# Performance work log

Measured on AMD Instinct MI355X. Metric: run time of the kernel, lower is better.

Reference implementation:

```python
import jax, jax.numpy as jnp
import numpy as np

ITERATION = 3
NEG = -2.0**16 + 1.0  # mask fill value from the torch code


def setup_inputs() -> dict:
    key = jax.random.key(0)
    k1, k2, k3, k4 = jax.random.split(key, 4)
    B, L, D_in, D_out, K = 1024, 512, 64, 64, 8
    low_capsule = jax.random.normal(k1, (B, L, D_in), dtype=jnp.float32)
    B_init = jax.random.normal(k2, (1, K, L), dtype=jnp.float32)
    S = jax.random.normal(k3, (D_in, D_out), dtype=jnp.float32)
    seq_len = jax.random.randint(k4, (B, 1), 1, L + 1, dtype=jnp.int32)
    return {"low_capsule": low_capsule, "B_init": B_init, "S": S, "seq_len": seq_len}


def _squash(x):
    # torch code sums squared norm over dim=1 (the capsule/max_k dim), keepdim
    sq = jnp.sum(jnp.square(x), axis=1, keepdims=True)
    scale = sq / (1.0 + sq) / jnp.sqrt(sq + 1e-9)
    return scale * x


def reference(low_capsule, B_init, S, seq_len):
    # low_capsule: [B, L, D_in], B_init: [1, K, L], S: [D_in, D_out], seq_len: [B, 1]
    Bsz, L, _ = low_capsule.shape
    K = B_init.shape[1]
    # sequence mask: [B, K, L] (seq_len tiled over K)
    mask = jnp.arange(L, dtype=seq_len.dtype)[None, None, :] < seq_len[:, :, None]
    mask = jnp.broadcast_to(mask, (Bsz, K, L))
    # bilinear projection is loop-invariant; compute once
    low_new = jnp.einsum('bld,do->blo', low_capsule, S)  # [B, L, D_out]
    B_mat = B_init
    high = None
    for _ in range(ITERATION):
        logits = jnp.where(mask, B_mat, NEG)               # [B, K, L]
        W = jax.nn.softmax(logits, axis=-1)                # masked softmax
        high = _squash(jnp.einsum('bkl,blo->bko', W, low_new))  # [B, K, D_out]
        B_delta = jnp.sum(jnp.einsum('bko,blo->bkl', high, low_new),
                          axis=0, keepdims=True)           # [1, K, L]
        B_mat = B_mat + B_delta
    return high
```

## Files before the change

kernel.cpp:

```cpp
#include <hip/hip_runtime.h>

#define NEG_FILL (-65535.0f)
#define NSLOT 32

typedef __attribute__((ext_vector_type(8))) short  short8;
typedef __attribute__((ext_vector_type(4))) float  floatx4;

__device__ inline unsigned short f2bf(float f) {
    unsigned u = __float_as_uint(f);
    u += 0x7FFFu + ((u >> 16) & 1u);
    return (unsigned short)(u >> 16);
}
__device__ inline float bf2f(unsigned short h) {
    return __uint_as_float(((unsigned)h) << 16);
}

__global__ __launch_bounds__(256) void k_init(const float* __restrict__ Binit,
                                              float* __restrict__ B0,
                                              float* __restrict__ slots) {
    int i = blockIdx.x * 256 + threadIdx.x;
    slots[i] = 0.f;
    if (i < 4096) B0[i] = Binit[i];
}

__global__ __launch_bounds__(256) void k_bred(const float* __restrict__ Bcur,
                                              float* __restrict__ Bnext,
                                              float* __restrict__ slots) {
    int i = blockIdx.x * 256 + threadIdx.x;
    float s = Bcur[i];
    #pragma unroll
    for (int j = 0; j < NSLOT; ++j) {
        s += slots[j * 4096 + i];
        slots[j * 4096 + i] = 0.f;
    }
    Bnext[i] = s;
}

__device__ __forceinline__ void softmax_to_WsT(
    const float* __restrict__ Bc, int sl, int lane, int g,
    float (*WsT)[8]) {
    #pragma unroll
    for (int kk = 0; kk < 2; ++kk) {
        const int k = g + (kk << 2);
        float v[8];
        float mx = NEG_FILL;
        #pragma unroll
        for (int j = 0; j < 8; ++j) {
            int l = lane + (j << 6);
            v[j] = (l < sl) ? Bc[(k << 9) + l] : NEG_FILL;
            mx = fmaxf(mx, v[j]);
        }
        #pragma unroll
        for (int off = 32; off; off >>= 1) mx = fmaxf(mx, __shfl_xor(mx, off));
        float s = 0.f;
        #pragma unroll
        for (int j = 0; j < 8; ++j) { v[j] = expf(v[j] - mx); s += v[j]; }
        #pragma unroll
        for (int off = 32; off; off >>= 1) s += __shfl_xor(s, off);
        const float inv = 1.0f / s;
        #pragma unroll
        for (int j = 0; j < 8; ++j) WsT[lane + (j << 6)][k] = v[j] * inv;
    }
}

__device__ __forceinline__ void delta_phase(
    const unsigned short* __restrict__ lnb, const unsigned short (*Hn)[64],
    float* __restrict__ slot, int g, int m, int q) {
    short8 afragH[2];
    #pragma unroll
    for (int oh = 0; oh < 2; ++oh) {
        short8 f = {0, 0, 0, 0, 0, 0, 0, 0};
        if (m < 8) f = *(const short8*)&Hn[m][oh * 32 + q * 8];
        afragH[oh] = f;
    }
    #pragma unroll
    for (int half = 0; half < 2; ++half) {
        short8 bf[4][2];
        #pragma unroll
        for (int t2 = 0; t2 < 4; ++t2) {
            const int lt = (g << 7) + (((half << 2) + t2) << 4);
            const unsigned short* p = &lnb[((lt + m) << 6) + q * 8];
            bf[t2][0] = *(const short8*)p;
            bf[t2][1] = *(const short8*)(p + 32);
        }
        #pragma unroll
        for (int t2 = 0; t2 < 4; ++t2) {
            const int lt = (g << 7) + (((half << 2) + t2) << 4);
            floatx4 acc = {0.f, 0.f, 0.f, 0.f};
            acc = __builtin_amdgcn_mfma_f32_16x16x32_bf16(afragH[0], bf[t2][0], acc, 0, 0, 0);
            acc = __builtin_amdgcn_mfma_f32_16x16x32_bf16(afragH[1], bf[t2][1], acc, 0, 0, 0);
            if (q < 2) {
                #pragma unroll
                for (int r = 0; r < 4; ++r)
                    atomicAdd(&slot[(q * 4 + r) * 512 + lt + m], acc[r]);
            }
        }
    }
}

__global__ __launch_bounds__(256, 4) void k_fused0(
    const float* __restrict__ low,
    const float* __restrict__ S,
    const float* __restrict__ Bc,
    float* __restrict__ slots,
    const int* __restrict__ seq_len,
    unsigned short* __restrict__ ln)
{
    __shared__ __align__(16) float WsT[512][8];
    __shared__ __align__(16) float Tpart[4][8][64];
    __shared__ __align__(16) float Tred[8][64];
    __shared__ __align__(16) unsigned short Hn[8][64];

    const int t = threadIdx.x, lane = t & 63, g = t >> 6, b = blockIdx.x;
    const int m = lane & 15, q = lane >> 4;
    const int sl = seq_len[b];
    const float* lowb = low + ((size_t)b << 15);
    unsigned short* lnb = ln + ((size_t)b << 15);

    softmax_to_WsT(Bc, sl, lane, g, WsT);
    __syncthreads();

    short8 sfrag[4][2];
    #pragma unroll
    for (int nt = 0; nt < 4; ++nt)
        #pragma unroll
        for (int dh = 0; dh < 2; ++dh) {
            short8 f;
            #pragma unroll
            for (int j = 0; j < 8; ++j) {
                int d = dh * 32 + q * 8 + j;
                f[j] = (short)f2bf(S[(d << 6) + nt * 16 + m]);
            }
            sfrag[nt][dh] = f;
        }

    float Tp[8][4];
    #pragma unroll
    for (int k = 0; k < 8; ++k)
        #pragma unroll
        for (int nt = 0; nt < 4; ++nt) Tp[k][nt] = 0.f;

    for (int tt = 0; tt < 8; ++tt) {
        const int lt = (g << 7) + (tt << 4);
        short8 afrag[2];
        #pragma unroll
        for (int dh = 0; dh < 2; ++dh) {
            const float4* p =
                (const float4*)&lowb[((lt + m) << 6) + dh * 32 + q * 8];
            float4 x0 = p[0], x1 = p[1];
            short8 f;
            f[0] = (short)f2bf(x0.x); f[1] = (short)f2bf(x0.y);
            f[2] = (short)f2bf(x0.z); f[3] = (short)f2bf(x0.w);
            f[4] = (short)f2bf(x1.x); f[5] = (short)f2bf(x1.y);
            f[6] = (short)f2bf(x1.z); f[7] = (short)f2bf(x1.w);
            afrag[dh] = f;
        }
        float lnr[4][4];
        #pragma unroll
        for (int nt = 0; nt < 4; ++nt) {
            floatx4 acc = {0.f, 0.f, 0.f, 0.f};
            acc = __builtin_amdgcn_mfma_f32_16x16x32_bf16(afrag[0], sfrag[nt][0], acc, 0, 0, 0);
            acc = __builtin_amdgcn_mfma_f32_16x16x32_bf16(afrag[1], sfrag[nt][1], acc, 0, 0, 0);
            #pragma unroll
            for (int r = 0; r < 4; ++r) {
                unsigned short hb = f2bf(acc[r]);
                lnb[((size_t)(lt + (q << 2) + r) << 6) + nt * 16 + m] = hb;
                lnr[r][nt] = bf2f(hb);
            }
        }
        #pragma unroll
        for (int r = 0; r < 4; ++r) {
            const int l = lt + (q << 2) + r;
            const float4 wa = *(const float4*)&WsT[l][0];
            const float4 wb = *(const float4*)&WsT[l][4];
            #pragma unroll
            for (int nt = 0; nt < 4; ++nt) {
                const float x = lnr[r][nt];
                Tp[0][nt] = fmaf(wa.x, x, Tp[0][nt]);
                Tp[1][nt] = fmaf(wa.y, x, Tp[1][nt]);
                Tp[2][nt] = fmaf(wa.z, x, Tp[2][nt]);
                Tp[3][nt] = fmaf(wa.w, x, Tp[3][nt]);
                Tp[4][nt] = fmaf(wb.x, x, Tp[4][nt]);
                Tp[5][nt] = fmaf(wb.y, x, Tp[5][nt]);
                Tp[6][nt] = fmaf(wb.z, x, Tp[6][nt]);
                Tp[7][nt] = fmaf(wb.w, x, Tp[7][nt]);
            }
        }
    }
    #pragma unroll
    for (int k = 0; k < 8; ++k)
        #pragma unroll
        for (int nt = 0; nt < 4; ++nt) {
            float v = Tp[k][nt];
            v += __shfl_xor(v, 16);
            v += __shfl_xor(v, 32);
            Tp[k][nt] = v;
        }
    #pragma unroll
    for (int k = 0; k < 8; ++k) Tpart[g][k][lane] = Tp[k][q];
    __syncthreads();

    #pragma unroll
    for (int idx = t; idx < 512; idx += 256) {
        float s = (&Tpart[0][0][0])[idx] + (&Tpart[1][0][0])[idx]
                + (&Tpart[2][0][0])[idx] + (&Tpart[3][0][0])[idx];
        (&Tred[0][0])[idx] = s;
    }
    __syncthreads();

    float sq = 0.f;
    #pragma unroll
    for (int k = 0; k < 8; ++k) { float x = Tred[k][lane]; sq = fmaf(x, x, sq); }
    const float scale = sq / (1.0f + sq) / sqrtf(sq + 1e-9f);
    Hn[g][lane]     = f2bf(scale * Tred[g][lane]);
    Hn[g + 4][lane] = f2bf(scale * Tred[g + 4][lane]);
    __syncthreads();

    delta_phase(lnb, Hn, slots + ((size_t)(b & (NSLOT - 1)) << 12), g, m, q);
}

__global__ __launch_bounds__(256, 4) void k_route2(
    const unsigned short* __restrict__ ln,
    const float* __restrict__ Bc,
    float* __restrict__ slots,
    const int* __restrict__ seq_len,
    float* __restrict__ out,
    int last)
{
    __shared__ __align__(16) float WsT[512][8];
    __shared__ __align__(16) float Tpart[4][8][64];
    __shared__ __align__(16) float Tred[8][64];
    __shared__ __align__(16) unsigned short Hn[8][64];

    const int t = threadIdx.x, lane = t & 63, g = t >> 6, b = blockIdx.x;
    const int m = lane & 15, q = lane >> 4;
    const int sl = seq_len[b];
    const unsigned short* lnb = ln + ((size_t)b << 15);

    softmax_to_WsT(Bc, sl, lane, g, WsT);
    __syncthreads();

    floatx4 Tacc[8];
    #pragma unroll
    for (int k = 0; k < 8; ++k) Tacc[k] = (floatx4){0.f, 0.f, 0.f, 0.f};
    const int l0 = g << 7;
    for (int ii = 0; ii < 4; ++ii) {
        uint2 u[8];
        #pragma unroll
        for (int j = 0; j < 8; ++j) {
            const int l = l0 + (ii << 5) + (j << 2) + q;
            u[j] = *(const uint2*)&lnb[(l << 6) + (m << 2)];
        }
        #pragma unroll
        for (int j = 0; j < 8; ++j) {
            const int l = l0 + (ii << 5) + (j << 2) + q;
            const float x0 = __uint_as_float(u[j].x << 16);
            const float x1 = __uint_as_float(u[j].x & 0xFFFF0000u);
            const float x2 = __uint_as_float(u[j].y << 16);
            const float x3 = __uint_as_float(u[j].y & 0xFFFF0000u);
            const float4 wa = *(const float4*)&WsT[l][0];
            const float4 wb = *(const float4*)&WsT[l][4];
#define TROW(K, WV)                                          \
            Tacc[K][0] = fmaf(WV, x0, Tacc[K][0]);           \
            Tacc[K][1] = fmaf(WV, x1, Tacc[K][1]);           \
            Tacc[K][2] = fmaf(WV, x2, Tacc[K][2]);           \
            Tacc[K][3] = fmaf(WV, x3, Tacc[K][3]);
            TROW(0, wa.x) TROW(1, wa.y) TROW(2, wa.z) TROW(3, wa.w)
            TROW(4, wb.x) TROW(5, wb.y) TROW(6, wb.z) TROW(7, wb.w)
#undef TROW
        }
    }
    #pragma unroll
    for (int k = 0; k < 8; ++k)
        #pragma unroll
        for (int j = 0; j < 4; ++j) {
            float v = Tacc[k][j];
            v += __shfl_xor(v, 16);
            v += __shfl_xor(v, 32);
            Tacc[k][j] = v;
        }
    if (q == 0) {
        #pragma unroll
        for (int k = 0; k < 8; ++k)
            *(float4*)&Tpart[g][k][m << 2] =
                make_float4(Tacc[k][0], Tacc[k][1], Tacc[k][2], Tacc[k][3]);
    }
    __syncthreads();

    #pragma unroll
    for (int idx = t; idx < 512; idx += 256) {
        float s = (&Tpart[0][0][0])[idx] + (&Tpart[1][0][0])[idx]
                + (&Tpart[2][0][0])[idx] + (&Tpart[3][0][0])[idx];
        (&Tred[0][0])[idx] = s;
    }
    __syncthreads();

    float sq = 0.f;
    #pragma unroll
    for (int k = 0; k < 8; ++k) { float x = Tred[k][lane]; sq = fmaf(x, x, sq); }
    const float scale = sq / (1.0f + sq) / sqrtf(sq + 1e-9f);
    const float hf0 = scale * Tred[g][lane];
    const float hf1 = scale * Tred[g + 4][lane];

    if (last) {
        out[(((size_t)b * 8 + g)     << 6) + lane] = hf0;
        out[(((size_t)b * 8 + g + 4) << 6) + lane] = hf1;
        return;
    }
    Hn[g][lane]     = f2bf(hf0);
    Hn[g + 4][lane] = f2bf(hf1);
    __syncthreads();

    delta_phase(lnb, Hn, slots + ((size_t)(b & (NSLOT - 1)) << 12), g, m, q);
}

__global__ __launch_bounds__(256) void k_copy4k(const float* __restrict__ src,
                                                float* __restrict__ dst) {
    int i = blockIdx.x * 256 + threadIdx.x;
    dst[i] = src[i];
}

__global__ __launch_bounds__(256, 4) void k_route(
    const float* __restrict__ low, const float* __restrict__ S,
    const float* __restrict__ Bcur, float* __restrict__ Bnext,
    const int* __restrict__ seq_len, float* __restrict__ out, int last)
{
    __shared__ float smemA[64 * 65];
    __shared__ float Spad[64][65];
    __shared__ float GT[64][8];
    __shared__ float Tred[8][64];
    float* WsT = smemA;
    float (*Tpart)[8][64] = (float (*)[8][64])smemA;
    float (*tile)[65]     = (float (*)[65])smemA;

    const int t = threadIdx.x, o = t & 63, g = t >> 6, b = blockIdx.x;
    const int sl = seq_len[b];
    const float* lowb = low + ((size_t)b << 15);

    #pragma unroll
    for (int i = 0; i < 16; ++i) {
        int idx = t + (i << 8);
        Spad[idx >> 6][idx & 63] = S[idx];
    }
    #pragma unroll
    for (int kk = 0; kk < 2; ++kk) {
        const int k = g + (kk << 2);
        float v[8];
        float mx = NEG_FILL;
        #pragma unroll
        for (int j = 0; j < 8; ++j) {
            int l = o + (j << 6);
            v[j] = (l < sl) ? Bcur[(k << 9) + l] : NEG_FILL;
            mx = fmaxf(mx, v[j]);
        }
        #pragma unroll
        for (int off = 32; off; off >>= 1) mx = fmaxf(mx, __shfl_xor(mx, off));
        float s = 0.f;
        #pragma unroll
        for (int j = 0; j < 8; ++j) { v[j] = expf(v[j] - mx); s += v[j]; }
        #pragma unroll
        for (int off = 32; off; off >>= 1) s += __shfl_xor(s, off);
        const float inv = 1.0f / s;
        #pragma unroll
        for (int j = 0; j < 8; ++j) WsT[((o + (j << 6)) << 3) + k] = v[j] * inv;
    }
    __syncthreads();

    float Ta[8];
    #pragma unroll
    for (int k = 0; k < 8; ++k) Ta[k] = 0.f;
    {
        const int l0 = g << 7;
        #pragma unroll 4
        for (int i = 0; i < 128; ++i) {
            const int l = l0 + i;
            const float x = lowb[(l << 6) + o];
            const float4 wa = *(const float4*)&WsT[(l << 3)];
            const float4 wb = *(const float4*)&WsT[(l << 3) + 4];
            Ta[0] = fmaf(wa.x, x, Ta[0]); Ta[1] = fmaf(wa.y, x, Ta[1]);
            Ta[2] = fmaf(wa.z, x, Ta[2]); Ta[3] = fmaf(wa.w, x, Ta[3]);
            Ta[4] = fmaf(wb.x, x, Ta[4]); Ta[5] = fmaf(wb.y, x, Ta[5]);
            Ta[6] = fmaf(wb.z, x, Ta[6]); Ta[7] = fmaf(wb.w, x, Ta[7]);
        }
    }
    __syncthreads();
    #pragma unroll
    for (int k = 0; k < 8; ++k) Tpart[g][k][o] = Ta[k];
    __syncthreads();

    float h0 = 0.f, h1 = 0.f;
    #pragma unroll
    for (int gg = 0; gg < 4; ++gg) { h0 += Tpart[gg][g][o]; h1 += Tpart[gg][g + 4][o]; }
    Tred[g][o] = h0; Tred[g + 4][o] = h1;
    __syncthreads();

    float hp0 = 0.f, hp1 = 0.f;
    #pragma unroll
    for (int d = 0; d < 64; ++d) {
        const float sv = Spad[d][o];
        hp0 = fmaf(Tred[g][d], sv, hp0);
        hp1 = fmaf(Tred[g + 4][d], sv, hp1);
    }
    __syncthreads();
    Tred[g][o] = hp0; Tred[g + 4][o] = hp1;
    __syncthreads();

    float sq = 0.f;
    #pragma unroll
    for (int k = 0; k < 8; ++k) { float x = Tred[k][o]; sq = fmaf(x, x, sq); }
    const float scale = sq / (1.0f + sq) / sqrtf(sq + 1e-9f);
    const float hf0 = scale * hp0;
    const float hf1 = scale * hp1;

    if (last) {
        out[(((size_t)b * 8 + g)     << 6) + o] = hf0;
        out[(((size_t)b * 8 + g + 4) << 6) + o] = hf1;
        return;
    }
    __syncthreads();
    Tred[g][o] = hf0; Tred[g + 4][o] = hf1;
    __syncthreads();

    float g0 = 0.f, g1 = 0.f;
    #pragma unroll
    for (int oo = 0; oo < 64; ++oo) {
        const float sv = Spad[o][oo];
        g0 = fmaf(Tred[g][oo], sv, g0);
        g1 = fmaf(Tred[g + 4][oo], sv, g1);
    }
    GT[o][g] = g0; GT[o][g + 4] = g1;
    __syncthreads();

    for (int c = 0; c < 8; ++c) {
        const int lc = c << 6;
        #pragma unroll
        for (int r = 0; r < 16; ++r) {
            const int lr = (g << 4) + r;
            tile[lr][o] = lowb[((lc + lr) << 6) + o];
        }
        __syncthreads();
        float a0 = 0.f, a1 = 0.f;
        #pragma unroll
        for (int d = 0; d < 64; ++d) {
            const float x = tile[o][d];
            a0 = fmaf(GT[d][g], x, a0);
            a1 = fmaf(GT[d][g + 4], x, a1);
        }
        atomicAdd(&Bnext[(g << 9) + lc + o], a0);
        atomicAdd(&Bnext[((g + 4) << 9) + lc + o], a1);
        __syncthreads();
    }
}

extern "C" void kernel_launch(void* const* d_in, const int* in_sizes, int n_in,
                              void* d_out, int out_size, void* d_ws, size_t ws_size,
                              hipStream_t stream) {
    const float* low   = (const float*)d_in[0];
    const float* Binit = (const float*)d_in[1];
    const float* S     = (const float*)d_in[2];
    const int*   seq   = (const int*)d_in[3];
    float* outp = (float*)d_out;

    const size_t LN_BYTES   = (size_t)1024 * 512 * 64 * 2;
    const size_t SLOT_BYTES = (size_t)NSLOT * 4096 * sizeof(float);
    const size_t NEED = LN_BYTES + SLOT_BYTES + 2 * 4096 * sizeof(float);

    if (ws_size >= NEED) {
        unsigned short* lnw = (unsigned short*)d_ws;
        float* slots = (float*)((char*)d_ws + LN_BYTES);
        float* B0 = slots + (size_t)NSLOT * 4096;
        float* B1 = B0 + 4096;

        k_init<<<(NSLOT * 4096) / 256, 256, 0, stream>>>(Binit, B0, slots);

        k_fused0<<<1024, 256, 0, stream>>>(low, S, B0, slots, seq, lnw);
        k_bred<<<16, 256, 0, stream>>>(B0, B1, slots);

        k_route2<<<1024, 256, 0, stream>>>(lnw, B1, slots, seq, outp, 0);
        k_bred<<<16, 256, 0, stream>>>(B1, B0, slots);

        k_route2<<<1024, 256, 0, stream>>>(lnw, B0, nullptr, seq, outp, 1);
    } else {
        float* B0 = (float*)d_ws;
        float* B1 = B0 + 4096;
        k_copy4k<<<16, 256, 0, stream>>>(Binit, B0);
        k_copy4k<<<16, 256, 0, stream>>>(B0, B1);
        k_route<<<1024, 256, 0, stream>>>(low, S, B0, B1, seq, outp, 0);
        k_copy4k<<<16, 256, 0, stream>>>(B1, B0);
        k_route<<<1024, 256, 0, stream>>>(low, S, B1, B0, seq, outp, 0);
        k_route<<<1024, 256, 0, stream>>>(low, S, B0, nullptr, seq, outp, 1);
    }
}
```

Measured before the change: 283.3 us.

## Split each batch row across two blocks and separate delta into its own kernel

Each batch row's routing work is now split across two blocks, each handling half of the sequence. Partial T sums are atomically accumulated into a global buffer that reuses the output array. The squash and delta MFMA phase moves into a separate k_delta kernel, and a final k_out kernel applies the squash. This doubles the block count and lowers per-block shared memory (launch bounds raised to 6) for better occupancy, at the cost of extra kernel launches, global atomics, and T-buffer zeroing traffic in k_bred.

After: 373.4 us. 1.32x slower.

```diff
diff --git a/kernel.cpp b/kernel.cpp
--- a/kernel.cpp
+++ b/kernel.cpp
@@ -15,17 +15,17 @@
     return __uint_as_float(((unsigned)h) << 16);
 }
 
-__global__ __launch_bounds__(256) void k_init(const float* __restrict__ Binit,
-                                              float* __restrict__ B0,
-                                              float* __restrict__ slots) {
+__global__ __launch_bounds__(256) void k_init(float* __restrict__ slots,
+                                              float* __restrict__ Tbuf) {
     int i = blockIdx.x * 256 + threadIdx.x;
-    slots[i] = 0.f;
-    if (i < 4096) B0[i] = Binit[i];
+    Tbuf[i] = 0.f;
+    if (i < NSLOT * 4096) slots[i] = 0.f;
 }
 
 __global__ __launch_bounds__(256) void k_bred(const float* __restrict__ Bcur,
                                               float* __restrict__ Bnext,
-                                              float* __restrict__ slots) {
+                                              float* __restrict__ slots,
+                                              float* __restrict__ Tbuf) {
     int i = blockIdx.x * 256 + threadIdx.x;
     float s = Bcur[i];
     #pragma unroll
@@ -34,10 +34,12 @@
         slots[j * 4096 + i] = 0.f;
     }
     Bnext[i] = s;
-}
-
-__device__ __forceinline__ void softmax_to_WsT(
-    const float* __restrict__ Bc, int sl, int lane, int g,
+    #pragma unroll 16
+    for (int j = 0; j < 128; ++j) Tbuf[j * 4096 + i] = 0.f;
+}
+
+__device__ __forceinline__ void softmax_half(
+    const float* __restrict__ Bc, int sl, int lane, int g, int half,
     float (*WsT)[8]) {
     #pragma unroll
     for (int kk = 0; kk < 2; ++kk) {
@@ -59,65 +61,30 @@
         for (int off = 32; off; off >>= 1) s += __shfl_xor(s, off);
         const float inv = 1.0f / s;
         #pragma unroll
-        for (int j = 0; j < 8; ++j) WsT[lane + (j << 6)][k] = v[j] * inv;
-    }
-}
-
-__device__ __forceinline__ void delta_phase(
-    const unsigned short* __restrict__ lnb, const unsigned short (*Hn)[64],
-    float* __restrict__ slot, int g, int m, int q) {
-    short8 afragH[2];
-    #pragma unroll
-    for (int oh = 0; oh < 2; ++oh) {
-        short8 f = {0, 0, 0, 0, 0, 0, 0, 0};
-        if (m < 8) f = *(const short8*)&Hn[m][oh * 32 + q * 8];
-        afragH[oh] = f;
-    }
-    #pragma unroll
-    for (int half = 0; half < 2; ++half) {
-        short8 bf[4][2];
-        #pragma unroll
-        for (int t2 = 0; t2 < 4; ++t2) {
-            const int lt = (g << 7) + (((half << 2) + t2) << 4);
-            const unsigned short* p = &lnb[((lt + m) << 6) + q * 8];
-            bf[t2][0] = *(const short8*)p;
-            bf[t2][1] = *(const short8*)(p + 32);
-        }
-        #pragma unroll
-        for (int t2 = 0; t2 < 4; ++t2) {
-            const int lt = (g << 7) + (((half << 2) + t2) << 4);
-            floatx4 acc = {0.f, 0.f, 0.f, 0.f};
-            acc = __builtin_amdgcn_mfma_f32_16x16x32_bf16(afragH[0], bf[t2][0], acc, 0, 0, 0);
-            acc = __builtin_amdgcn_mfma_f32_16x16x32_bf16(afragH[1], bf[t2][1], acc, 0, 0, 0);
-            if (q < 2) {
-                #pragma unroll
-                for (int r = 0; r < 4; ++r)
-                    atomicAdd(&slot[(q * 4 + r) * 512 + lt + m], acc[r]);
-            }
-        }
-    }
-}
-
-__global__ __launch_bounds__(256, 4) void k_fused0(
+        for (int j = 0; j < 4; ++j)
+            WsT[lane + (j << 6)][k] = v[(half << 2) + j] * inv;
+    }
+}
+
+__global__ __launch_bounds__(256, 6) void k_F0(
     const float* __restrict__ low,
     const float* __restrict__ S,
     const float* __restrict__ Bc,
-    float* __restrict__ slots,
     const int* __restrict__ seq_len,
-    unsigned short* __restrict__ ln)
+    unsigned short* __restrict__ ln,
+    float* __restrict__ Tbuf)
 {
-    __shared__ __align__(16) float WsT[512][8];
+    __shared__ __align__(16) float WsT[256][8];
     __shared__ __align__(16) float Tpart[4][8][64];
-    __shared__ __align__(16) float Tred[8][64];
-    __shared__ __align__(16) unsigned short Hn[8][64];
-
-    const int t = threadIdx.x, lane = t & 63, g = t >> 6, b = blockIdx.x;
+
+    const int t = threadIdx.x, lane = t & 63, g = t >> 6;
+    const int b = blockIdx.x >> 1, half = blockIdx.x & 1;
     const int m = lane & 15, q = lane >> 4;
     const int sl = seq_len[b];
-    const float* lowb = low + ((size_t)b << 15);
-    unsigned short* lnb = ln + ((size_t)b << 15);
-
-    softmax_to_WsT(Bc, sl, lane, g, WsT);
+    const float* lowb = low + ((size_t)b << 15) + ((size_t)half << 14);
+    unsigned short* lnb = ln + ((size_t)b << 15) + ((size_t)half << 14);
+
+    softmax_half(Bc, sl, lane, g, half, WsT);
     __syncthreads();
 
     short8 sfrag[4][2];
@@ -140,8 +107,8 @@
         #pragma unroll
         for (int nt = 0; nt < 4; ++nt) Tp[k][nt] = 0.f;
 
-    for (int tt = 0; tt < 8; ++tt) {
-        const int lt = (g << 7) + (tt << 4);
+    for (int tt = 0; tt < 4; ++tt) {
+        const int lt = (g << 6) + (tt << 4);
         short8 afrag[2];
         #pragma unroll
         for (int dh = 0; dh < 2; ++dh) {
@@ -155,18 +122,13 @@
             f[6] = (short)f2bf(x1.z); f[7] = (short)f2bf(x1.w);
             afrag[dh] = f;
         }
-        float lnr[4][4];
+        floatx4 accs[4];
         #pragma unroll
         for (int nt = 0; nt < 4; ++nt) {
             floatx4 acc = {0.f, 0.f, 0.f, 0.f};
             acc = __builtin_amdgcn_mfma_f32_16x16x32_bf16(afrag[0], sfrag[nt][0], acc, 0, 0, 0);
             acc = __builtin_amdgcn_mfma_f32_16x16x32_bf16(afrag[1], sfrag[nt][1], acc, 0, 0, 0);
-            #pragma unroll
-            for (int r = 0; r < 4; ++r) {
-                unsigned short hb = f2bf(acc[r]);
-                lnb[((size_t)(lt + (q << 2) + r) << 6) + nt * 16 + m] = hb;
-                lnr[r][nt] = bf2f(hb);
-            }
+            accs[nt] = acc;
         }
         #pragma unroll
         for (int r = 0; r < 4; ++r) {
@@ -175,7 +137,9 @@
             const float4 wb = *(const float4*)&WsT[l][4];
             #pragma unroll
             for (int nt = 0; nt < 4; ++nt) {
-                const float x = lnr[r][nt];
+                unsigned short hb = f2bf(accs[nt][r]);
+                lnb[((size_t)l << 6) + nt * 16 + m] = hb;
+                const float x = bf2f(hb);
                 Tp[0][nt] = fmaf(wa.x, x, Tp[0][nt]);
                 Tp[1][nt] = fmaf(wa.y, x, Tp[1][nt]);
                 Tp[2][nt] = fmaf(wa.z, x, Tp[2][nt]);
@@ -204,47 +168,33 @@
     for (int idx = t; idx < 512; idx += 256) {
         float s = (&Tpart[0][0][0])[idx] + (&Tpart[1][0][0])[idx]
                 + (&Tpart[2][0][0])[idx] + (&Tpart[3][0][0])[idx];
-        (&Tred[0][0])[idx] = s;
-    }
-    __syncthreads();
-
-    float sq = 0.f;
-    #pragma unroll
-    for (int k = 0; k < 8; ++k) { float x = Tred[k][lane]; sq = fmaf(x, x, sq); }
-    const float scale = sq / (1.0f + sq) / sqrtf(sq + 1e-9f);
-    Hn[g][lane]     = f2bf(scale * Tred[g][lane]);
-    Hn[g + 4][lane] = f2bf(scale * Tred[g + 4][lane]);
-    __syncthreads();
-
-    delta_phase(lnb, Hn, slots + ((size_t)(b & (NSLOT - 1)) << 12), g, m, q);
-}
-
-__global__ __launch_bounds__(256, 4) void k_route2(
+        atomicAdd(&Tbuf[((size_t)b << 9) + idx], s);
+    }
+}
+
+__global__ __launch_bounds__(256, 6) void k_T(
     const unsigned short* __restrict__ ln,
     const float* __restrict__ Bc,
-    float* __restrict__ slots,
     const int* __restrict__ seq_len,
-    float* __restrict__ out,
-    int last)
+    float* __restrict__ Tbuf)
 {
-    __shared__ __align__(16) float WsT[512][8];
+    __shared__ __align__(16) float WsT[256][8];
     __shared__ __align__(16) float Tpart[4][8][64];
-    __shared__ __align__(16) float Tred[8][64];
-    __shared__ __align__(16) unsigned short Hn[8][64];
-
-    const int t = threadIdx.x, lane = t & 63, g = t >> 6, b = blockIdx.x;
+
+    const int t = threadIdx.x, lane = t & 63, g = t >> 6;
+    const int b = blockIdx.x >> 1, half = blockIdx.x & 1;
     const int m = lane & 15, q = lane >> 4;
     const int sl = seq_len[b];
-    const unsigned short* lnb = ln + ((size_t)b << 15);
-
-    softmax_to_WsT(Bc, sl, lane, g, WsT);
+    const unsigned short* lnb = ln + ((size_t)b << 15) + ((size_t)half << 14);
+
+    softmax_half(Bc, sl, lane, g, half, WsT);
     __syncthreads();
 
     floatx4 Tacc[8];
     #pragma unroll
     for (int k = 0; k < 8; ++k) Tacc[k] = (floatx4){0.f, 0.f, 0.f, 0.f};
-    const int l0 = g << 7;
-    for (int ii = 0; ii < 4; ++ii) {
+    const int l0 = g << 6;
+    for (int ii = 0; ii < 2; ++ii) {
         uint2 u[8];
         #pragma unroll
         for (int j = 0; j < 8; ++j) {
@@ -291,27 +241,79 @@
     for (int idx = t; idx < 512; idx += 256) {
         float s = (&Tpart[0][0][0])[idx] + (&Tpart[1][0][0])[idx]
                 + (&Tpart[2][0][0])[idx] + (&Tpart[3][0][0])[idx];
-        (&Tred[0][0])[idx] = s;
-    }
-    __syncthreads();
-
-    float sq = 0.f;
-    #pragma unroll
-    for (int k = 0; k < 8; ++k) { float x = Tred[k][lane]; sq = fmaf(x, x, sq); }
+        atomicAdd(&Tbuf[((size_t)b << 9) + idx], s);
+    }
+}
+
+__global__ __launch_bounds__(256, 6) void k_delta(
+    const unsigned short* __restrict__ ln,
+    const float* __restrict__ Tbuf,
+    float* __restrict__ slots)
+{
+    __shared__ __align__(16) float Tl[512];
+    __shared__ __align__(16) unsigned short Hn[8][64];
+
+    const int t = threadIdx.x, lane = t & 63, g = t >> 6;
+    const int b = blockIdx.x >> 1, half = blockIdx.x & 1;
+    const int m = lane & 15, q = lane >> 4;
+    const unsigned short* lnb = ln + ((size_t)b << 15);
+    float* slot = slots + ((size_t)(b & (NSLOT - 1)) << 12);
+
+    Tl[t]       = Tbuf[((size_t)b << 9) + t];
+    Tl[t + 256] = Tbuf[((size_t)b << 9) + t + 256];
+    __syncthreads();
+    if (t < 64) {
+        float sq = 0.f;
+        #pragma unroll
+        for (int k = 0; k < 8; ++k) { float x = Tl[(k << 6) + t]; sq = fmaf(x, x, sq); }
+        const float scale = sq / (1.0f + sq) / sqrtf(sq + 1e-9f);
+        #pragma unroll
+        for (int k = 0; k < 8; ++k) Hn[k][t] = f2bf(scale * Tl[(k << 6) + t]);
+    }
+    __syncthreads();
+
+    short8 aH[2];
+    #pragma unroll
+    for (int oh = 0; oh < 2; ++oh) {
+        short8 f = {0, 0, 0, 0, 0, 0, 0, 0};
+        if (m < 8) f = *(const short8*)&Hn[m][oh * 32 + q * 8];
+        aH[oh] = f;
+    }
+    short8 bf[4][2];
+    #pragma unroll
+    for (int t2 = 0; t2 < 4; ++t2) {
+        const int lt = (half << 8) + (g << 6) + (t2 << 4);
+        const unsigned short* p = &lnb[((lt + m) << 6) + q * 8];
+        bf[t2][0] = *(const short8*)p;
+        bf[t2][1] = *(const short8*)(p + 32);
+    }
+    #pragma unroll
+    for (int t2 = 0; t2 < 4; ++t2) {
+        const int lt = (half << 8) + (g << 6) + (t2 << 4);
+        floatx4 acc = {0.f, 0.f, 0.f, 0.f};
+        acc = __builtin_amdgcn_mfma_f32_16x16x32_bf16(aH[0], bf[t2][0], acc, 0, 0, 0);
+        acc = __builtin_amdgcn_mfma_f32_16x16x32_bf16(aH[1], bf[t2][1], acc, 0, 0, 0);
+        if (q < 2) {
+            #pragma unroll
+            for (int r = 0; r < 4; ++r)
+                atomicAdd(&slot[((q << 2) + r) * 512 + lt + m], acc[r]);
+        }
+    }
+}
+
+__global__ __launch_bounds__(256) void k_out(float* T_io) {
+    const int idx = blockIdx.x * 256 + threadIdx.x;
+    const int b = idx >> 6, o = idx & 63;
+    float v[8]; float sq = 0.f;
+    #pragma unroll
+    for (int k = 0; k < 8; ++k) {
+        v[k] = T_io[((size_t)b << 9) + (k << 6) + o];
+        sq = fmaf(v[k], v[k], sq);
+    }
     const float scale = sq / (1.0f + sq) / sqrtf(sq + 1e-9f);
-    const float hf0 = scale * Tred[g][lane];
-    const float hf1 = scale * Tred[g + 4][lane];
-
-    if (last) {
-        out[(((size_t)b * 8 + g)     << 6) + lane] = hf0;
-        out[(((size_t)b * 8 + g + 4) << 6) + lane] = hf1;
-        return;
-    }
-    Hn[g][lane]     = f2bf(hf0);
-    Hn[g + 4][lane] = f2bf(hf1);
-    __syncthreads();
-
-    delta_phase(lnb, Hn, slots + ((size_t)(b & (NSLOT - 1)) << 12), g, m, q);
+    #pragma unroll
+    for (int k = 0; k < 8; ++k)
+        T_io[((size_t)b << 9) + (k << 6) + o] = scale * v[k];
 }
 
 __global__ __launch_bounds__(256) void k_copy4k(const float* __restrict__ src,
@@ -470,16 +472,20 @@
         float* slots = (float*)((char*)d_ws + LN_BYTES);
         float* B0 = slots + (size_t)NSLOT * 4096;
         float* B1 = B0 + 4096;
-
-        k_init<<<(NSLOT * 4096) / 256, 256, 0, stream>>>(Binit, B0, slots);
-
-        k_fused0<<<1024, 256, 0, stream>>>(low, S, B0, slots, seq, lnw);
-        k_bred<<<16, 256, 0, stream>>>(B0, B1, slots);
-
-        k_route2<<<1024, 256, 0, stream>>>(lnw, B1, slots, seq, outp, 0);
-        k_bred<<<16, 256, 0, stream>>>(B1, B0, slots);
-
-        k_route2<<<1024, 256, 0, stream>>>(lnw, B0, nullptr, seq, outp, 1);
+        float* T  = outp;
+
+        k_init<<<2048, 256, 0, stream>>>(slots, T);
+
+        k_F0<<<2048, 256, 0, stream>>>(low, S, Binit, seq, lnw, T);
+        k_delta<<<2048, 256, 0, stream>>>(lnw, T, slots);
+        k_bred<<<16, 256, 0, stream>>>(Binit, B1, slots, T);
+
+        k_T<<<2048, 256, 0, stream>>>(lnw, B1, seq, T);
+        k_delta<<<2048, 256, 0, stream>>>(lnw, T, slots);
+        k_bred<<<16, 256, 0, stream>>>(B1, B0, slots, T);
+
+        k_T<<<2048, 256, 0, stream>>>(lnw, B0, seq, T);
+        k_out<<<256, 256, 0, stream>>>(T);
     } else {
         float* B0 = (float*)d_ws;
         float* B1 = B0 + 4096;
```

## Prefetch input tiles and skip masked-out rows in routing accumulation

Applied to the files above, without the earlier changes.

In the projection kernel, the next 16-row tile of the low capsule input is now register-prefetched so its global loads overlap the current tile's MFMA work. The weighted accumulation is skipped for tiles that lie entirely past the sequence length, since their softmax weights are zero. In the later routing-iteration kernel, bf16 row chunks are double-buffered across two register sets, and only chunks that overlap the valid sequence length are loaded and accumulated. This removes wasted memory traffic and FMAs on masked positions, at the cost of higher register pressure and possible divergence.

Result: slower. 331.7 us (+17.1%).

```diff
diff --git a/kernel.cpp b/kernel.cpp
--- a/kernel.cpp
+++ b/kernel.cpp
@@ -13,6 +13,14 @@
 }
 __device__ inline float bf2f(unsigned short h) {
     return __uint_as_float(((unsigned)h) << 16);
+}
+__device__ __forceinline__ short8 pack8(float4 a, float4 b) {
+    short8 f;
+    f[0] = (short)f2bf(a.x); f[1] = (short)f2bf(a.y);
+    f[2] = (short)f2bf(a.z); f[3] = (short)f2bf(a.w);
+    f[4] = (short)f2bf(b.x); f[5] = (short)f2bf(b.y);
+    f[6] = (short)f2bf(b.z); f[7] = (short)f2bf(b.w);
+    return f;
 }
 
 __global__ __launch_bounds__(256) void k_init(const float* __restrict__ Binit,
@@ -117,6 +125,10 @@
     const float* lowb = low + ((size_t)b << 15);
     unsigned short* lnb = ln + ((size_t)b << 15);
 
+    const float* rp0 = &lowb[(((g << 7) + m) << 6) + (q << 3)];
+    float4 cx0 = *(const float4*)rp0,        cx1 = *(const float4*)(rp0 + 4);
+    float4 cx2 = *(const float4*)(rp0 + 32), cx3 = *(const float4*)(rp0 + 36);
+
     softmax_to_WsT(Bc, sl, lane, g, WsT);
     __syncthreads();
 
@@ -140,21 +152,19 @@
         #pragma unroll
         for (int nt = 0; nt < 4; ++nt) Tp[k][nt] = 0.f;
 
+    float4 nx0, nx1, nx2, nx3;
+    #pragma unroll
     for (int tt = 0; tt < 8; ++tt) {
         const int lt = (g << 7) + (tt << 4);
+        if (tt < 7) {
+            const float* rp = &lowb[((lt + 16 + m) << 6) + (q << 3)];
+            nx0 = *(const float4*)rp;        nx1 = *(const float4*)(rp + 4);
+            nx2 = *(const float4*)(rp + 32); nx3 = *(const float4*)(rp + 36);
+        }
         short8 afrag[2];
-        #pragma unroll
-        for (int dh = 0; dh < 2; ++dh) {
-            const float4* p =
-                (const float4*)&lowb[((lt + m) << 6) + dh * 32 + q * 8];
-            float4 x0 = p[0], x1 = p[1];
-            short8 f;
-            f[0] = (short)f2bf(x0.x); f[1] = (short)f2bf(x0.y);
-            f[2] = (short)f2bf(x0.z); f[3] = (short)f2bf(x0.w);
-            f[4] = (short)f2bf(x1.x); f[5] = (short)f2bf(x1.y);
-            f[6] = (short)f2bf(x1.z); f[7] = (short)f2bf(x1.w);
-            afrag[dh] = f;
-        }
+        afrag[0] = pack8(cx0, cx1);
+        afrag[1] = pack8(cx2, cx3);
+
         float lnr[4][4];
         #pragma unroll
         for (int nt = 0; nt < 4; ++nt) {
@@ -168,24 +178,27 @@
                 lnr[r][nt] = bf2f(hb);
             }
         }
-        #pragma unroll
-        for (int r = 0; r < 4; ++r) {
-            const int l = lt + (q << 2) + r;
-            const float4 wa = *(const float4*)&WsT[l][0];
-            const float4 wb = *(const float4*)&WsT[l][4];
+        if (lt < sl) {
             #pragma unroll
-            for (int nt = 0; nt < 4; ++nt) {
-                const float x = lnr[r][nt];
-                Tp[0][nt] = fmaf(wa.x, x, Tp[0][nt]);
-                Tp[1][nt] = fmaf(wa.y, x, Tp[1][nt]);
-                Tp[2][nt] = fmaf(wa.z, x, Tp[2][nt]);
-                Tp[3][nt] = fmaf(wa.w, x, Tp[3][nt]);
-                Tp[4][nt] = fmaf(wb.x, x, Tp[4][nt]);
-                Tp[5][nt] = fmaf(wb.y, x, Tp[5][nt]);
-                Tp[6][nt] = fmaf(wb.z, x, Tp[6][nt]);
-                Tp[7][nt] = fmaf(wb.w, x, Tp[7][nt]);
+            for (int r = 0; r < 4; ++r) {
+                const int l = lt + (q << 2) + r;
+                const float4 wa = *(const float4*)&WsT[l][0];
+                const float4 wb = *(const float4*)&WsT[l][4];
+                #pragma unroll
+                for (int nt = 0; nt < 4; ++nt) {
+                    const float x = lnr[r][nt];
+                    Tp[0][nt] = fmaf(wa.x, x, Tp[0][nt]);
+                    Tp[1][nt] = fmaf(wa.y, x, Tp[1][nt]);
+                    Tp[2][nt] = fmaf(wa.z, x, Tp[2][nt]);
+                    Tp[3][nt] = fmaf(wa.w, x, Tp[3][nt]);
+                    Tp[4][nt] = fmaf(wb.x, x, Tp[4][nt]);
+                    Tp[5][nt] = fmaf(wb.y, x, Tp[5][nt]);
+                    Tp[6][nt] = fmaf(wb.z, x, Tp[6][nt]);
+                    Tp[7][nt] = fmaf(wb.w, x, Tp[7][nt]);
+                }
             }
         }
+        cx0 = nx0; cx1 = nx1; cx2 = nx2; cx3 = nx3;
     }
     #pragma unroll
     for (int k = 0; k < 8; ++k)
@@ -244,32 +257,53 @@
     #pragma unroll
     for (int k = 0; k < 8; ++k) Tacc[k] = (floatx4){0.f, 0.f, 0.f, 0.f};
     const int l0 = g << 7;
-    for (int ii = 0; ii < 4; ++ii) {
-        uint2 u[8];
-        #pragma unroll
-        for (int j = 0; j < 8; ++j) {
-            const int l = l0 + (ii << 5) + (j << 2) + q;
-            u[j] = *(const uint2*)&lnb[(l << 6) + (m << 2)];
-        }
-        #pragma unroll
-        for (int j = 0; j < 8; ++j) {
-            const int l = l0 + (ii << 5) + (j << 2) + q;
-            const float x0 = __uint_as_float(u[j].x << 16);
-            const float x1 = __uint_as_float(u[j].x & 0xFFFF0000u);
-            const float x2 = __uint_as_float(u[j].y << 16);
-            const float x3 = __uint_as_float(u[j].y & 0xFFFF0000u);
-            const float4 wa = *(const float4*)&WsT[l][0];
-            const float4 wb = *(const float4*)&WsT[l][4];
+    const int rem = sl - l0;
+    int nact = (rem <= 0) ? 0 : ((rem + 31) >> 5);
+    if (nact > 4) nact = 4;
+
+    uint2 uA[8], uB[8];
+
+#define LOADB(II, U)                                                      \
+    { _Pragma("unroll")                                                   \
+      for (int j = 0; j < 8; ++j) {                                       \
+          const int l = l0 + ((II) << 5) + (j << 2) + q;                  \
+          U[j] = *(const uint2*)&lnb[(l << 6) + (m << 2)];                \
+      } }
+
+#define COMPB(II, U)                                                      \
+    { _Pragma("unroll")                                                   \
+      for (int j = 0; j < 8; ++j) {                                       \
+          const int l = l0 + ((II) << 5) + (j << 2) + q;                  \
+          const float x0 = __uint_as_float(U[j].x << 16);                 \
+          const float x1 = __uint_as_float(U[j].x & 0xFFFF0000u);         \
+          const float x2 = __uint_as_float(U[j].y << 16);                 \
+          const float x3 = __uint_as_float(U[j].y & 0xFFFF0000u);         \
+          const float4 wa = *(const float4*)&WsT[l][0];                   \
+          const float4 wb = *(const float4*)&WsT[l][4];                   \
+          TROW(0, wa.x) TROW(1, wa.y) TROW(2, wa.z) TROW(3, wa.w)         \
+          TROW(4, wb.x) TROW(5, wb.y) TROW(6, wb.z) TROW(7, wb.w)         \
+      } }
+
 #define TROW(K, WV)                                          \
             Tacc[K][0] = fmaf(WV, x0, Tacc[K][0]);           \
             Tacc[K][1] = fmaf(WV, x1, Tacc[K][1]);           \
             Tacc[K][2] = fmaf(WV, x2, Tacc[K][2]);           \
             Tacc[K][3] = fmaf(WV, x3, Tacc[K][3]);
-            TROW(0, wa.x) TROW(1, wa.y) TROW(2, wa.z) TROW(3, wa.w)
-            TROW(4, wb.x) TROW(5, wb.y) TROW(6, wb.z) TROW(7, wb.w)
+
+    if (nact > 0) {
+        LOADB(0, uA);
+        if (nact > 1) LOADB(1, uB);
+        COMPB(0, uA);
+        if (nact > 2) LOADB(2, uA);
+        if (nact > 1) COMPB(1, uB);
+        if (nact > 3) LOADB(3, uB);
+        if (nact > 2) COMPB(2, uA);
+        if (nact > 3) COMPB(3, uB);
+    }
 #undef TROW
-        }
-    }
+#undef COMPB
+#undef LOADB
+
     #pragma unroll
     for (int k = 0; k < 8; ++k)
         #pragma unroll
```

## Double block size to 512 threads and skip masked L chunks in routing

Applied to the files above, without the earlier changes.

Moves k_fused0 and k_route2 from 256 to 512 threads per block, so each wave owns one capsule k for the softmax and 64 sequence positions instead of 128. The cross-wave reduction grows to eight partials. k_route2 also skips 32-row chunks that lie beyond seq_len, since their softmax weights are zero, which cuts loads of the bf16 projection for short sequences. In exchange it raises per-SM register and LDS pressure and doubles the wave count per block; the launch-bounds occupancy target goes from 4 to 8.

After: 407.5 us. 43.8% more time.

```diff
diff --git a/kernel.cpp b/kernel.cpp
--- a/kernel.cpp
+++ b/kernel.cpp
@@ -13,6 +13,14 @@
 }
 __device__ inline float bf2f(unsigned short h) {
     return __uint_as_float(((unsigned)h) << 16);
+}
+__device__ __forceinline__ short8 pack8(float4 a, float4 b) {
+    short8 f;
+    f[0] = (short)f2bf(a.x); f[1] = (short)f2bf(a.y);
+    f[2] = (short)f2bf(a.z); f[3] = (short)f2bf(a.w);
+    f[4] = (short)f2bf(b.x); f[5] = (short)f2bf(b.y);
+    f[6] = (short)f2bf(b.z); f[7] = (short)f2bf(b.w);
+    return f;
 }
 
 __global__ __launch_bounds__(256) void k_init(const float* __restrict__ Binit,
@@ -36,34 +44,30 @@
     Bnext[i] = s;
 }
 
-__device__ __forceinline__ void softmax_to_WsT(
-    const float* __restrict__ Bc, int sl, int lane, int g,
+__device__ __forceinline__ void softmax_one_k(
+    const float* __restrict__ Bc, int sl, int lane, int k,
     float (*WsT)[8]) {
-    #pragma unroll
-    for (int kk = 0; kk < 2; ++kk) {
-        const int k = g + (kk << 2);
-        float v[8];
-        float mx = NEG_FILL;
-        #pragma unroll
-        for (int j = 0; j < 8; ++j) {
-            int l = lane + (j << 6);
-            v[j] = (l < sl) ? Bc[(k << 9) + l] : NEG_FILL;
-            mx = fmaxf(mx, v[j]);
-        }
-        #pragma unroll
-        for (int off = 32; off; off >>= 1) mx = fmaxf(mx, __shfl_xor(mx, off));
-        float s = 0.f;
-        #pragma unroll
-        for (int j = 0; j < 8; ++j) { v[j] = expf(v[j] - mx); s += v[j]; }
-        #pragma unroll
-        for (int off = 32; off; off >>= 1) s += __shfl_xor(s, off);
-        const float inv = 1.0f / s;
-        #pragma unroll
-        for (int j = 0; j < 8; ++j) WsT[lane + (j << 6)][k] = v[j] * inv;
-    }
-}
-
-__device__ __forceinline__ void delta_phase(
+    float v[8];
+    float mx = NEG_FILL;
+    #pragma unroll
+    for (int j = 0; j < 8; ++j) {
+        int l = lane + (j << 6);
+        v[j] = (l < sl) ? Bc[(k << 9) + l] : NEG_FILL;
+        mx = fmaxf(mx, v[j]);
+    }
+    #pragma unroll
+    for (int off = 32; off; off >>= 1) mx = fmaxf(mx, __shfl_xor(mx, off));
+    float s = 0.f;
+    #pragma unroll
+    for (int j = 0; j < 8; ++j) { v[j] = expf(v[j] - mx); s += v[j]; }
+    #pragma unroll
+    for (int off = 32; off; off >>= 1) s += __shfl_xor(s, off);
+    const float inv = 1.0f / s;
+    #pragma unroll
+    for (int j = 0; j < 8; ++j) WsT[lane + (j << 6)][k] = v[j] * inv;
+}
+
+__device__ __forceinline__ void delta_phase8(
     const unsigned short* __restrict__ lnb, const unsigned short (*Hn)[64],
     float* __restrict__ slot, int g, int m, int q) {
     short8 afragH[2];
@@ -73,32 +77,29 @@
         if (m < 8) f = *(const short8*)&Hn[m][oh * 32 + q * 8];
         afragH[oh] = f;
     }
-    #pragma unroll
-    for (int half = 0; half < 2; ++half) {
-        short8 bf[4][2];
-        #pragma unroll
-        for (int t2 = 0; t2 < 4; ++t2) {
-            const int lt = (g << 7) + (((half << 2) + t2) << 4);
-            const unsigned short* p = &lnb[((lt + m) << 6) + q * 8];
-            bf[t2][0] = *(const short8*)p;
-            bf[t2][1] = *(const short8*)(p + 32);
-        }
-        #pragma unroll
-        for (int t2 = 0; t2 < 4; ++t2) {
-            const int lt = (g << 7) + (((half << 2) + t2) << 4);
-            floatx4 acc = {0.f, 0.f, 0.f, 0.f};
-            acc = __builtin_amdgcn_mfma_f32_16x16x32_bf16(afragH[0], bf[t2][0], acc, 0, 0, 0);
-            acc = __builtin_amdgcn_mfma_f32_16x16x32_bf16(afragH[1], bf[t2][1], acc, 0, 0, 0);
-            if (q < 2) {
-                #pragma unroll
-                for (int r = 0; r < 4; ++r)
-                    atomicAdd(&slot[(q * 4 + r) * 512 + lt + m], acc[r]);
-            }
-        }
-    }
-}
-
-__global__ __launch_bounds__(256, 4) void k_fused0(
+    short8 bf[4][2];
+    #pragma unroll
+    for (int t2 = 0; t2 < 4; ++t2) {
+        const int lt = (g << 6) + (t2 << 4);
+        const unsigned short* p = &lnb[((lt + m) << 6) + q * 8];
+        bf[t2][0] = *(const short8*)p;
+        bf[t2][1] = *(const short8*)(p + 32);
+    }
+    #pragma unroll
+    for (int t2 = 0; t2 < 4; ++t2) {
+        const int lt = (g << 6) + (t2 << 4);
+        floatx4 acc = {0.f, 0.f, 0.f, 0.f};
+        acc = __builtin_amdgcn_mfma_f32_16x16x32_bf16(afragH[0], bf[t2][0], acc, 0, 0, 0);
+        acc = __builtin_amdgcn_mfma_f32_16x16x32_bf16(afragH[1], bf[t2][1], acc, 0, 0, 0);
+        if (q < 2) {
+            #pragma unroll
+            for (int r = 0; r < 4; ++r)
+                atomicAdd(&slot[(q * 4 + r) * 512 + lt + m], acc[r]);
+        }
+    }
+}
+
+__global__ __launch_bounds__(512, 8) void k_fused0(
     const float* __restrict__ low,
     const float* __restrict__ S,
     const float* __restrict__ Bc,
@@ -107,7 +108,7 @@
     unsigned short* __restrict__ ln)
 {
     __shared__ __align__(16) float WsT[512][8];
-    __shared__ __align__(16) float Tpart[4][8][64];
+    __shared__ __align__(16) float Tpart[8][8][64];
     __shared__ __align__(16) float Tred[8][64];
     __shared__ __align__(16) unsigned short Hn[8][64];
 
@@ -117,7 +118,7 @@
     const float* lowb = low + ((size_t)b << 15);
     unsigned short* lnb = ln + ((size_t)b << 15);
 
-    softmax_to_WsT(Bc, sl, lane, g, WsT);
+    softmax_one_k(Bc, sl, lane, g, WsT);
     __syncthreads();
 
     short8 sfrag[4][2];
@@ -140,20 +141,14 @@
         #pragma unroll
         for (int nt = 0; nt < 4; ++nt) Tp[k][nt] = 0.f;
 
-    for (int tt = 0; tt < 8; ++tt) {
-        const int lt = (g << 7) + (tt << 4);
+    for (int tt = 0; tt < 4; ++tt) {
+        const int lt = (g << 6) + (tt << 4);
         short8 afrag[2];
         #pragma unroll
         for (int dh = 0; dh < 2; ++dh) {
             const float4* p =
                 (const float4*)&lowb[((lt + m) << 6) + dh * 32 + q * 8];
-            float4 x0 = p[0], x1 = p[1];
-            short8 f;
-            f[0] = (short)f2bf(x0.x); f[1] = (short)f2bf(x0.y);
-            f[2] = (short)f2bf(x0.z); f[3] = (short)f2bf(x0.w);
-            f[4] = (short)f2bf(x1.x); f[5] = (short)f2bf(x1.y);
-            f[6] = (short)f2bf(x1.z); f[7] = (short)f2bf(x1.w);
-            afrag[dh] = f;
+            afrag[dh] = pack8(p[0], p[1]);
         }
         float lnr[4][4];
         #pragma unroll
@@ -200,10 +195,11 @@
     for (int k = 0; k < 8; ++k) Tpart[g][k][lane] = Tp[k][q];
     __syncthreads();
 
-    #pragma unroll
-    for (int idx = t; idx < 512; idx += 256) {
-        float s = (&Tpart[0][0][0])[idx] + (&Tpart[1][0][0])[idx]
-                + (&Tpart[2][0][0])[idx] + (&Tpart[3][0][0])[idx];
+    {
+        const int idx = t;
+        float s = 0.f;
+        #pragma unroll
+        for (int gg = 0; gg < 8; ++gg) s += (&Tpart[gg][0][0])[idx];
         (&Tred[0][0])[idx] = s;
     }
     __syncthreads();
@@ -212,14 +208,13 @@
     #pragma unroll
     for (int k = 0; k < 8; ++k) { float x = Tred[k][lane]; sq = fmaf(x, x, sq); }
     const float scale = sq / (1.0f + sq) / sqrtf(sq + 1e-9f);
-    Hn[g][lane]     = f2bf(scale * Tred[g][lane]);
-    Hn[g + 4][lane] = f2bf(scale * Tred[g + 4][lane]);
-    __syncthreads();
-
-    delta_phase(lnb, Hn, slots + ((size_t)(b & (NSLOT - 1)) << 12), g, m, q);
-}
-
-__global__ __launch_bounds__(256, 4) void k_route2(
+    Hn[g][lane] = f2bf(scale * Tred[g][lane]);
+    __syncthreads();
+
+    delta_phase8(lnb, Hn, slots + ((size_t)(b & (NSLOT - 1)) << 12), g, m, q);
+}
+
+__global__ __launch_bounds__(512, 8) void k_route2(
     const unsigned short* __restrict__ ln,
     const float* __restrict__ Bc,
     float* __restrict__ slots,
@@ -228,7 +223,7 @@
     int last)
 {
     __shared__ __align__(16) float WsT[512][8];
-    __shared__ __align__(16) float Tpart[4][8][64];
+    __shared__ __align__(16) float Tpart[8][8][64];
     __shared__ __align__(16) float Tred[8][64];
     __shared__ __align__(16) unsigned short Hn[8][64];
 
@@ -237,14 +232,18 @@
     const int sl = seq_len[b];
     const unsigned short* lnb = ln + ((size_t)b << 15);
 
-    softmax_to_WsT(Bc, sl, lane, g, WsT);
+    softmax_one_k(Bc, sl, lane, g, WsT);
     __syncthreads();
 
     floatx4 Tacc[8];
     #pragma unroll
     for (int k = 0; k < 8; ++k) Tacc[k] = (floatx4){0.f, 0.f, 0.f, 0.f};
-    const int l0 = g << 7;
-    for (int ii = 0; ii < 4; ++ii) {
+    const int l0 = g << 6;
+    const int rem = sl - l0;
+    int nact = (rem <= 0) ? 0 : ((rem + 31) >> 5);
+    if (nact > 2) nact = 2;
+
+    for (int ii = 0; ii < nact; ++ii) {
         uint2 u[8];
         #pragma unroll
         for (int j = 0; j < 8; ++j) {
@@ -287,10 +286,11 @@
     }
     __syncthreads();
 
-    #pragma unroll
-    for (int idx = t; idx < 512; idx += 256) {
-        float s = (&Tpart[0][0][0])[idx] + (&Tpart[1][0][0])[idx]
-                + (&Tpart[2][0][0])[idx] + (&Tpart[3][0][0])[idx];
+    {
+        const int idx = t;
+        float s = 0.f;
+        #pragma unroll
+        for (int gg = 0; gg < 8; ++gg) s += (&Tpart[gg][0][0])[idx];
         (&Tred[0][0])[idx] = s;
     }
     __syncthreads();
@@ -299,19 +299,16 @@
     #pragma unroll
     for (int k = 0; k < 8; ++k) { float x = Tred[k][lane]; sq = fmaf(x, x, sq); }
     const float scale = sq / (1.0f + sq) / sqrtf(sq + 1e-9f);
-    const float hf0 = scale * Tred[g][lane];
-    const float hf1 = scale * Tred[g + 4][lane];
+    const float hf = scale * Tred[g][lane];
 
     if (last) {
-        out[(((size_t)b * 8 + g)     << 6) + lane] = hf0;
-        out[(((size_t)b * 8 + g + 4) << 6) + lane] = hf1;
+        out[(((size_t)b * 8 + g) << 6) + lane] = hf;
         return;
     }
-    Hn[g][lane]     = f2bf(hf0);
-    Hn[g + 4][lane] = f2bf(hf1);
-    __syncthreads();
-
-    delta_phase(lnb, Hn, slots + ((size_t)(b & (NSLOT - 1)) << 12), g, m, q);
+    Hn[g][lane] = f2bf(hf);
+    __syncthreads();
+
+    delta_phase8(lnb, Hn, slots + ((size_t)(b & (NSLOT - 1)) << 12), g, m, q);
 }
 
 __global__ __launch_bounds__(256) void k_copy4k(const float* __restrict__ src,
@@ -473,13 +470,13 @@
 
         k_init<<<(NSLOT * 4096) / 256, 256, 0, stream>>>(Binit, B0, slots);
 
-        k_fused0<<<1024, 256, 0, stream>>>(low, S, B0, slots, seq, lnw);
+        k_fused0<<<1024, 512, 0, stream>>>(low, S, B0, slots, seq, lnw);
         k_bred<<<16, 256, 0, stream>>>(B0, B1, slots);
 
-        k_route2<<<1024, 256, 0, stream>>>(lnw, B1, slots, seq, outp, 0);
+        k_route2<<<1024, 512, 0, stream>>>(lnw, B1, slots, seq, outp, 0);
         k_bred<<<16, 256, 0, stream>>>(B1, B0, slots);
 
-        k_route2<<<1024, 256, 0, stream>>>(lnw, B0, nullptr, seq, outp, 1);
+        k_route2<<<1024, 512, 0, stream>>>(lnw, B0, nullptr, seq, outp, 1);
     } else {
         float* B0 = (float*)d_ws;
         float* B1 = B0 + 4096;
```
